# Kernel tuning notes

Hardware: AMD Instinct MI355X
Metric: run time of the kernel (lower is better)

## Reference

```python
import jax, jax.numpy as jnp
import numpy as np

N, E, R, H, KG, CIN, HID, OUT = 50000, 800000, 8, 4, 128, 256, 128, 128


def leaky(x, s=0.01):
    return jnp.where(x > 0, x, s * x)


def rgat(x, src, dst, etype, W, q, k, b, heads, n_nodes):
    # W: [R, Cin, H*C]; PyG computes bmm(x_e, W[etype]) per edge; equivalent and
    # cheaper: transform all nodes under every relation, then gather per edge.
    D = W.shape[-1]
    C = D // heads
    hr = jnp.einsum('nc,rcd->rnd', x, W)          # [R, N, D]
    out_j = hr[etype, src]                         # [E, D] messages (source)
    out_i = hr[etype, dst]                         # [E, D] targets
    a = leaky(out_i @ q + out_j @ k, 0.2)          # [E, H] additive self-attention
    amax = jax.ops.segment_max(a, dst, num_segments=n_nodes)   # per-dst max
    ex = jnp.exp(a - amax[dst])
    denom = jax.ops.segment_sum(ex, dst, num_segments=n_nodes)
    alpha = ex / denom[dst]                        # segment softmax across relations
    msg = alpha[:, :, None] * out_j.reshape(-1, heads, C)
    agg = jax.ops.segment_sum(msg, dst, num_segments=n_nodes)  # [N, H, C]
    return agg.reshape(n_nodes, D) + b             # concat heads + bias


def setup_inputs() -> dict:
    key = jax.random.key(0)
    ks = jax.random.split(key, 24)
    s = 0.05
    inp = {
        'kg_emb': jax.random.normal(ks[0], (N, KG), jnp.float32),
        'ccle': jax.random.normal(ks[1], (N, 4), jnp.float32),
        'node_id': jnp.arange(N, dtype=jnp.int32),
        'edge_index': jax.random.randint(ks[2], (2, E), 0, N),
        'edge_type': jax.random.randint(ks[3], (E,), 0, R),
        'ccle_w1': jax.random.normal(ks[4], (4, 32), jnp.float32) * s,
        'ccle_b1': jnp.zeros((32,), jnp.float32),
        'ccle_w2': jax.random.normal(ks[5], (32, 128), jnp.float32) * s,
        'ccle_b2': jnp.zeros((128,), jnp.float32),
        'W1': jax.random.normal(ks[6], (R, CIN, HID), jnp.float32) * s,
        'q1': jax.random.normal(ks[7], (HID, H), jnp.float32) * s,
        'k1': jax.random.normal(ks[8], (HID, H), jnp.float32) * s,
        'b1': jnp.zeros((HID,), jnp.float32),
        'W2': jax.random.normal(ks[9], (R, HID, OUT), jnp.float32) * s,
        'q2': jax.random.normal(ks[10], (OUT, H), jnp.float32) * s,
        'k2': jax.random.normal(ks[11], (OUT, H), jnp.float32) * s,
        'b2': jnp.zeros((OUT,), jnp.float32),
        'skip_w1': jax.random.normal(ks[12], (CIN, HID), jnp.float32) * s,
        'skip_b1': jnp.zeros((HID,), jnp.float32),
        'skip_w2': jax.random.normal(ks[13], (HID, OUT), jnp.float32) * s,
        'skip_b2': jnp.zeros((OUT,), jnp.float32),
    }
    return inp


def reference(kg_emb, ccle, node_id, edge_index, edge_type,
              ccle_w1, ccle_b1, ccle_w2, ccle_b2,
              W1, q1, k1, b1, W2, q2, k2, b2,
              skip_w1, skip_b1, skip_w2, skip_b2):
    src, dst = edge_index[0], edge_index[1]
    # OmicsLayer encoder on ccle features
    ccle_out = leaky(ccle @ ccle_w1 + ccle_b1) @ ccle_w2 + ccle_b2  # [N,128]
    x_in = jnp.concatenate([kg_emb[node_id], ccle_out[node_id]], axis=1)  # [N,256]
    x = rgat(x_in, src, dst, edge_type, W1, q1, k1, b1, H, N)
    x = leaky(x)  # dropout p=0
    x = rgat(x, src, dst, edge_type, W2, q2, k2, b2, H, N)
    skip = leaky(x_in @ skip_w1 + skip_b1) @ skip_w2 + skip_b2
    x = leaky(x + skip)
    return x
```

## Files before the change

### kernel.cpp

```cpp
#include <hip/hip_runtime.h>
#include <hip/hip_bf16.h>

#define RREL 8
#define HEADS 4
#define DH 128
#define CIN1 256
#define BN 144
#define CSP2 132

typedef unsigned short ushortT;
typedef __attribute__((ext_vector_type(8))) short short8;
typedef __attribute__((ext_vector_type(4))) float f32x4;

__device__ __forceinline__ float lrelu(float x, float s) { return x > 0.f ? x : s * x; }

__device__ __forceinline__ float bf2f(unsigned short u) {
    return __uint_as_float(((unsigned)u) << 16);
}
__device__ __forceinline__ unsigned short f2bf(float f) {
    unsigned u = __float_as_uint(f);
    return (unsigned short)((u + 0x7fffu + ((u >> 16) & 1u)) >> 16);
}

__device__ __forceinline__ void glds16(const ushortT* g, ushortT* l) {
    __builtin_amdgcn_global_load_lds(
        (const __attribute__((address_space(1))) unsigned int*)g,
        (__attribute__((address_space(3))) unsigned int*)l, 16, 0, 0);
}

__global__ __launch_bounds__(256)
void encoder_kernel(const float* __restrict__ kg, const float* __restrict__ ccle,
                    const int* __restrict__ node_id,
                    const float* __restrict__ w1, const float* __restrict__ b1,
                    const float* __restrict__ w2, const float* __restrict__ b2,
                    ushortT* __restrict__ xb, int N)
{
    __shared__ float w1s[4 * 32], b1s[32];
    __shared__ float hs[64][36];
    int tid = threadIdx.x;
    if (tid < 128) w1s[tid] = w1[tid];
    if (tid < 32) b1s[tid] = b1[tid];

    int d0 = tid & 63;
    int w = tid >> 6;
    float w2c0[32], w2c1[32];
    #pragma unroll 8
    for (int j = 0; j < 32; j++) {
        w2c0[j] = w2[j * 128 + d0];
        w2c1[j] = w2[j * 128 + d0 + 64];
    }
    float bb0 = b2[d0], bb1 = b2[d0 + 64];
    int chunk = blockIdx.x * 64;
    __syncthreads();

    {
        int ln = tid >> 2;
        int n = chunk + ln;
        if (n < N) {
            int nid = node_id[n];
            float c0 = ccle[nid * 4 + 0], c1 = ccle[nid * 4 + 1];
            float c2 = ccle[nid * 4 + 2], c3 = ccle[nid * 4 + 3];
            int jb = (tid & 3) * 8;
            #pragma unroll
            for (int jj = 0; jj < 8; jj++) {
                int j = jb + jj;
                float h = fmaf(c0, w1s[j], fmaf(c1, w1s[32 + j],
                          fmaf(c2, w1s[64 + j], fmaf(c3, w1s[96 + j], b1s[j]))));
                hs[ln][j] = lrelu(h, 0.01f);
            }
        }
    }
    __syncthreads();

    for (int it = 0; it < 16; it++) {
        int ln = it * 4 + w;
        int gn = chunk + ln;
        if (gn >= N) continue;
        int nid = node_id[gn];
        ushortT* xrow = xb + (long)gn * CIN1;
        xrow[d0]      = f2bf(kg[(long)nid * 128 + d0]);
        xrow[d0 + 64] = f2bf(kg[(long)nid * 128 + d0 + 64]);
        float o0 = bb0, o1 = bb1;
        const float4* hp = (const float4*)hs[ln];
        #pragma unroll
        for (int v = 0; v < 8; v++) {
            float4 hv = hp[v];
            o0 = fmaf(hv.x, w2c0[v * 4 + 0], o0);
            o1 = fmaf(hv.x, w2c1[v * 4 + 0], o1);
            o0 = fmaf(hv.y, w2c0[v * 4 + 1], o0);
            o1 = fmaf(hv.y, w2c1[v * 4 + 1], o1);
            o0 = fmaf(hv.z, w2c0[v * 4 + 2], o0);
            o1 = fmaf(hv.z, w2c1[v * 4 + 2], o1);
            o0 = fmaf(hv.w, w2c0[v * 4 + 3], o0);
            o1 = fmaf(hv.w, w2c1[v * 4 + 3], o1);
        }
        xrow[128 + d0]      = f2bf(o0);
        xrow[128 + d0 + 64] = f2bf(o1);
    }
}

__global__ __launch_bounds__(256)
void wtrans_kernel(const float* __restrict__ W, const float* __restrict__ q,
                   const float* __restrict__ kv, const float* __restrict__ SW,
                   ushortT* __restrict__ WT, int K)
{
    long o = (long)blockIdx.x * 256 + threadIdx.x;
    long total = (long)9 * BN * K;
    if (o >= total) return;
    int k = (int)(o % K);
    long t = o / K;
    int d = (int)(t % BN);
    int r = (int)(t / BN);
    float v = 0.f;
    if (r < 8) {
        const float* Wr = W + ((long)r * K + k) * 128;
        if (d < 128) v = Wr[d];
        else if (d < 132) {
            int h = d - 128; float s = 0.f;
            for (int c = 0; c < 128; c++) s += Wr[c] * q[c * 4 + h];
            v = s;
        } else if (d < 136) {
            int h = d - 132; float s = 0.f;
            for (int c = 0; c < 128; c++) s += Wr[c] * kv[c * 4 + h];
            v = s;
        }
    } else if (d < 128) {
        v = SW[(long)k * 128 + d];
    }
    WT[o] = f2bf(v);
}

__global__ __launch_bounds__(256, 4)
void mfma_gemm(const ushortT* __restrict__ A, const ushortT* __restrict__ Askip,
               const ushortT* __restrict__ WT, ushortT* __restrict__ hrC,
               float* __restrict__ aqkout, const float* __restrict__ bskip,
               void* __restrict__ skipout, int skipf32, int actskip,
               int M, int K)
{
    __shared__ ushortT smem[128 * 64 + BN * 64];
    ushortT* As = smem;
    ushortT* Bs = smem + 128 * 64;
    int tid = threadIdx.x;
    int lane = tid & 63, w = tid >> 6;
    int l15 = lane & 15, lhi = lane >> 4;

    int nwg = gridDim.x;
    int orig = blockIdx.x;
    int qq = nwg >> 3, rrem = nwg & 7;
    int xcd = orig & 7, o8 = orig >> 3;
    int bid = (xcd < rrem ? xcd * (qq + 1) : rrem * (qq + 1) + (xcd - rrem) * qq) + o8;

    int r = bid % 9;
    int m0 = (bid / 9) * 128;
    const ushortT* Ab = (r < 8) ? A : Askip;
    const ushortT* Wb = WT + (long)r * BN * K;
    int wbase = (tid >> 6) << 6;
    f32x4 acc[2][9] = {};

    for (int k0 = 0; k0 < K; k0 += 64) {
        #pragma unroll
        for (int it = 0; it < 4; it++) {
            int idx = it * 256 + tid;
            int row = idx >> 3;
            int ko = ((idx ^ (idx >> 3)) & 7) * 8;
            glds16(Ab + (long)(m0 + row) * K + k0 + ko,
                   As + (it * 256 + wbase) * 8);
        }
        #pragma unroll
        for (int it = 0; it < 4; it++) {
            int idx = it * 256 + tid;
            int row = idx >> 3;
            int ko = ((idx ^ (idx >> 3)) & 7) * 8;
            glds16(Wb + (long)row * K + k0 + ko,
                   Bs + (it * 256 + wbase) * 8);
        }
        if (tid < 128) {
            int idx = 1024 + tid;
            int row = idx >> 3;
            int ko = ((idx ^ (idx >> 3)) & 7) * 8;
            glds16(Wb + (long)row * K + k0 + ko,
                   Bs + (1024 + wbase) * 8);
        }
        __syncthreads();
        #pragma unroll
        for (int kk = 0; kk < 64; kk += 32) {
            int xoro = ((((kk >> 3) + lhi) ^ (l15 & 7)) << 3);
            short8 af0 = *(const short8*)(As + (w * 32 + l15) * 64 + xoro);
            short8 af1 = *(const short8*)(As + (w * 32 + 16 + l15) * 64 + xoro);
            #pragma unroll
            for (int j = 0; j < 9; j++) {
                short8 bf8 = *(const short8*)(Bs + (j * 16 + l15) * 64 + xoro);
                acc[0][j] = __builtin_amdgcn_mfma_f32_16x16x32_bf16(af0, bf8, acc[0][j], 0, 0, 0);
                acc[1][j] = __builtin_amdgcn_mfma_f32_16x16x32_bf16(af1, bf8, acc[1][j], 0, 0, 0);
            }
        }
        __syncthreads();
    }

    if (r < 8 && l15 < 8) {
        #pragma unroll
        for (int i = 0; i < 2; i++)
            #pragma unroll
            for (int g = 0; g < 4; g++) {
                int row = w * 32 + i * 16 + lhi * 4 + g;
                if (m0 + row < M)
                    aqkout[((long)r * M + m0 + row) * 8 + l15] = acc[i][8][g];
            }
    }

    ushortT* Cs = smem;
    #pragma unroll
    for (int i = 0; i < 2; i++)
        #pragma unroll
        for (int j = 0; j < 8; j++) {
            int row = w * 32 + i * 16 + lhi * 4;
            int col = j * 16 + l15;
            #pragma unroll
            for (int g = 0; g < 4; g++)
                Cs[(row + g) * CSP2 + col] = f2bf(acc[i][j][g]);
        }
    __syncthreads();
    #pragma unroll
    for (int it = 0; it < 8; it++) {
        int idx = it * 2048 + tid * 8;
        int row = idx >> 7, col = idx & 127;
        if (m0 + row >= M) continue;
        const ushortT* cp = Cs + row * CSP2 + col;
        if (r < 8) {
            long gofs = ((long)r * M + m0 + row) * DH + col;
            *(uint4*)(hrC + gofs) = *(const uint4*)cp;
        } else {
            float v[8];
            #pragma unroll
            for (int u = 0; u < 8; u++) {
                float x = bf2f(cp[u]) + bskip[col + u];
                if (actskip) x = lrelu(x, 0.01f);
                v[u] = x;
            }
            long gofs = (long)(m0 + row) * DH + col;
            if (skipf32) {
                *(float4*)((float*)skipout + gofs)     = make_float4(v[0], v[1], v[2], v[3]);
                *(float4*)((float*)skipout + gofs + 4) = make_float4(v[4], v[5], v[6], v[7]);
            } else {
                uint4 pk;
                pk.x = (unsigned)f2bf(v[0]) | ((unsigned)f2bf(v[1]) << 16);
                pk.y = (unsigned)f2bf(v[2]) | ((unsigned)f2bf(v[3]) << 16);
                pk.z = (unsigned)f2bf(v[4]) | ((unsigned)f2bf(v[5]) << 16);
                pk.w = (unsigned)f2bf(v[6]) | ((unsigned)f2bf(v[7]) << 16);
                *(uint4*)((ushortT*)skipout + gofs) = pk;
            }
        }
    }
}

__global__ __launch_bounds__(256)
void hist_kernel(const int* __restrict__ dst, int* __restrict__ deg, int E)
{
    int e = blockIdx.x * 256 + threadIdx.x;
    if (e < E) atomicAdd(&deg[dst[e]], 1);
}

#define SCAN_BLK 1024
__global__ __launch_bounds__(256)
void scan1_kernel(const int* __restrict__ deg, int* __restrict__ excl,
                  int* __restrict__ bsum, int n)
{
    __shared__ int ts[256];
    int b0 = blockIdx.x * SCAN_BLK;
    int tid = threadIdx.x;
    int v[4]; int s = 0;
    #pragma unroll
    for (int i = 0; i < 4; i++) {
        int idx = b0 + tid * 4 + i;
        v[i] = (idx < n) ? deg[idx] : 0;
        s += v[i];
    }
    ts[tid] = s;
    __syncthreads();
    for (int off = 1; off < 256; off <<= 1) {
        int t = (tid >= off) ? ts[tid - off] : 0;
        __syncthreads();
        ts[tid] += t;
        __syncthreads();
    }
    int ex = ts[tid] - s;
    #pragma unroll
    for (int i = 0; i < 4; i++) {
        int idx = b0 + tid * 4 + i;
        if (idx < n) excl[idx] = ex;
        ex += v[i];
    }
    if (tid == 255) bsum[blockIdx.x] = ts[255];
}

__global__ void scan2_kernel(int* __restrict__ bsum, int nb)
{
    if (threadIdx.x == 0 && blockIdx.x == 0) {
        int a = 0;
        for (int i = 0; i < nb; i++) { int t = bsum[i]; bsum[i] = a; a += t; }
    }
}

__global__ __launch_bounds__(256)
void scan3_kernel(int* __restrict__ rowptr, const int* __restrict__ bsum,
                  int* __restrict__ cursor, int n, int E)
{
    int idx = blockIdx.x * 256 + threadIdx.x;
    if (idx < n) {
        int v = rowptr[idx] + bsum[idx / SCAN_BLK];
        rowptr[idx] = v;
        cursor[idx] = v;
    }
    if (idx == 0) rowptr[n] = E;
}

__global__ __launch_bounds__(256)
void scatter_kernel(const int* __restrict__ src, const int* __restrict__ dst,
                    const int* __restrict__ et, int* __restrict__ cursor,
                    int* __restrict__ srcs, int* __restrict__ ets, int E)
{
    int e = blockIdx.x * 256 + threadIdx.x;
    if (e >= E) return;
    int d = dst[e];
    int pos = atomicAdd(&cursor[d], 1);
    srcs[pos] = src[e];
    ets[pos] = et[e];
}

template<typename CT, bool ADDS>
__global__ __launch_bounds__(256)
void fused_agg(const int* __restrict__ rowptr, const int* __restrict__ srcs,
               const int* __restrict__ ets, const float* __restrict__ aqk,
               const ushortT* __restrict__ hr, const float* __restrict__ bias,
               const float* __restrict__ adds, void* __restrict__ outp,
               int N, int act)
{
    __shared__ ushortT hrb[4][16][128];
    __shared__ float pbuf[4][16][4];
    int w = threadIdx.x >> 6, lane = threadIdx.x & 63;
    int d = blockIdx.x * 4 + w;
    if (d >= N) return;
    int beg = rowptr[d], end = rowptr[d + 1];
    int el = lane & 15, hq = lane >> 4;
    float m = -1e30f, den = 0.f, o0 = 0.f, o1 = 0.f;

    for (int base = beg; base < end; base += 16) {
        int nchunk = end - base; if (nchunk > 16) nchunk = 16;
        int s = 0, t = 0;
        float a = -1e30f;
        if (el < nchunk) {
            s = srcs[base + el];
            t = ets[base + el];
            a = lrelu(aqk[((long)t * N + d) * 8 + hq]
                    + aqk[((long)t * N + s) * 8 + 4 + hq], 0.2f);
        }
        float v = a;
        v = fmaxf(v, __shfl_xor(v, 1));
        v = fmaxf(v, __shfl_xor(v, 2));
        v = fmaxf(v, __shfl_xor(v, 4));
        v = fmaxf(v, __shfl_xor(v, 8));
        float mn = fmaxf(m, v);
        float scale = __expf(m - mn);
        m = mn;
        float p = (el < nchunk) ? __expf(a - mn) : 0.f;
        pbuf[w][el][hq] = p;
        float ps = p;
        ps += __shfl_xor(ps, 1);
        ps += __shfl_xor(ps, 2);
        ps += __shfl_xor(ps, 4);
        ps += __shfl_xor(ps, 8);
        den = den * scale + ps;
        #pragma unroll
        for (int pass = 0; pass < 4; pass++) {
            int rj = pass * 4 + (lane >> 4);
            int sj = __shfl(s, rj);
            int tj = __shfl(t, rj);
            if (rj < nchunk) {
                uint4 hv = *(const uint4*)(hr + ((long)tj * N + sj) * DH + (lane & 15) * 8);
                *(uint4*)&hrb[w][rj][(lane & 15) * 8] = hv;
            }
        }
        o0 *= scale; o1 *= scale;
        asm volatile("s_waitcnt lgkmcnt(0)" ::: "memory");
        for (int j = 0; j < nchunk; j++) {
            float pj = pbuf[w][j][hq];
            unsigned hv = *(const unsigned*)&hrb[w][j][lane * 2];
            o0 = fmaf(pj, bf2f((ushortT)hv), o0);
            o1 = fmaf(pj, bf2f((ushortT)(hv >> 16)), o1);
        }
    }
    float inv = (den > 0.f) ? 1.f / den : 0.f;
    o0 *= inv; o1 *= inv;
    if (bias) { o0 += bias[2 * lane]; o1 += bias[2 * lane + 1]; }
    if constexpr (ADDS) {
        float2 sv = *(const float2*)(adds + (long)d * DH + lane * 2);
        o0 += sv.x; o1 += sv.y;
    }
    if (act) { o0 = lrelu(o0, 0.01f); o1 = lrelu(o1, 0.01f); }
    if constexpr (sizeof(CT) == 2) {
        unsigned pk = (unsigned)f2bf(o0) | ((unsigned)f2bf(o1) << 16);
        ((unsigned*)outp)[(long)d * 64 + lane] = pk;
    } else {
        *(float2*)((float*)outp + (long)d * DH + lane * 2) = make_float2(o0, o1);
    }
}

__global__ __launch_bounds__(256)
void fill_report(float* __restrict__ out, float v, long total)
{
    long i = (long)blockIdx.x * 256 + threadIdx.x;
    if (i < total) out[i] = v;
}

extern "C" void kernel_launch(void* const* d_in, const int* in_sizes, int n_in,
                              void* d_out, int out_size, void* d_ws, size_t ws_size,
                              hipStream_t stream)
{
    const float* kg      = (const float*)d_in[0];
    const float* ccle    = (const float*)d_in[1];
    const int*   node_id = (const int*)d_in[2];
    const int*   eidx    = (const int*)d_in[3];
    const int*   etype   = (const int*)d_in[4];
    const float* cw1 = (const float*)d_in[5];
    const float* cb1 = (const float*)d_in[6];
    const float* cw2 = (const float*)d_in[7];
    const float* cb2 = (const float*)d_in[8];
    const float* W1  = (const float*)d_in[9];
    const float* q1  = (const float*)d_in[10];
    const float* k1  = (const float*)d_in[11];
    const float* b1  = (const float*)d_in[12];
    const float* W2  = (const float*)d_in[13];
    const float* q2  = (const float*)d_in[14];
    const float* k2  = (const float*)d_in[15];
    const float* b2  = (const float*)d_in[16];
    const float* sw1 = (const float*)d_in[17];
    const float* sb1 = (const float*)d_in[18];
    const float* sw2 = (const float*)d_in[19];
    const float* sb2 = (const float*)d_in[20];

    const int N = in_sizes[2];
    const int E = in_sizes[4];
    const int* src = eidx;
    const int* dst = eidx + E;

    dim3 blk(256);
    long nd = (long)N * 128;
    int nd_blocks = (int)((nd + 255) / 256);
    int eb = (E + 255) / 256;

    const long WTN = (long)9 * BN * 256;
    size_t need = (size_t)N * (256 + 128 + 128 + 1024) * 2 + (size_t)WTN * 2
                + (size_t)N * 64 * 4 + (size_t)N * 128 * 4
                + ((size_t)3 * N + 257 + 2 * (size_t)E) * 4;
    if (ws_size < need) {
        fill_report<<<nd_blocks, blk, 0, stream>>>((float*)d_out,
            (float)(double)(ws_size >> 20), nd);
        return;
    }
    ushortT* xb  = (ushortT*)d_ws;
    ushortT* x1b = xb + (long)N * CIN1;
    ushortT* s1b = x1b + (long)N * DH;
    ushortT* hr  = s1b + (long)N * DH;
    ushortT* WT  = hr + (long)RREL * N * DH;
    float* aqk   = (float*)(WT + WTN);
    float* s2    = aqk + (long)N * 64;
    int* rowptr  = (int*)(s2 + (long)N * DH);
    int* cursor  = rowptr + (N + 1);
    int* deg     = cursor + N;
    int* bsum    = deg + N;
    int* srcs    = bsum + 256;
    int* ets     = srcs + E;

    int nb = (N + SCAN_BLK - 1) / SCAN_BLK;
    int fgrid = (N + 3) / 4;
    int mblocks = (N + 127) / 128;
    dim3 ggrid(mblocks * 9);

    encoder_kernel<<<(N + 63) / 64, blk, 0, stream>>>(kg, ccle, node_id,
        cw1, cb1, cw2, cb2, xb, N);

    hipMemsetAsync(deg, 0, (size_t)N * sizeof(int), stream);
    hist_kernel<<<eb, blk, 0, stream>>>(dst, deg, E);
    scan1_kernel<<<nb, blk, 0, stream>>>(deg, rowptr, bsum, N);
    scan2_kernel<<<1, 64, 0, stream>>>(bsum, nb);
    scan3_kernel<<<(N + 255) / 256, blk, 0, stream>>>(rowptr, bsum, cursor, N, E);
    scatter_kernel<<<eb, blk, 0, stream>>>(src, dst, etype, cursor, srcs, ets, E);

    wtrans_kernel<<<(int)(((long)9 * BN * CIN1 + 255) / 256), blk, 0, stream>>>(
        W1, q1, k1, sw1, WT, CIN1);
    mfma_gemm<<<ggrid, blk, 0, stream>>>(xb, xb, WT, hr, aqk, sb1, s1b,
        0, 1, N, CIN1);
    fused_agg<ushortT, false><<<fgrid, blk, 0, stream>>>(rowptr, srcs, ets,
        aqk, hr, b1, nullptr, x1b, N, 1);

    wtrans_kernel<<<(int)(((long)9 * BN * DH + 255) / 256), blk, 0, stream>>>(
        W2, q2, k2, sw2, WT, DH);
    mfma_gemm<<<ggrid, blk, 0, stream>>>(x1b, s1b, WT, hr, aqk, sb2, s2,
        1, 0, N, DH);
    fused_agg<float, true><<<fgrid, blk, 0, stream>>>(rowptr, srcs, ets,
        aqk, hr, b2, s2, (float*)d_out, N, 1);
}
```

Measured before the change: 365.4 us.

## Accumulate gathered messages in registers instead of staging through LDS

The fused aggregation kernel no longer stages the 16 gathered source rows and their softmax weights in shared memory. Each lane now loads four edges' 8-column slices straight into registers and accumulates eight partial sums. The four edge groups are combined with cross-lane shuffles at the end, and 16 lanes write vectorized outputs. This removes LDS traffic and the serial per-edge inner loop, and issues all gathers before the softmax math so load latency can overlap it, at the cost of more registers and a final shuffle reduction.

```diff
diff --git a/kernel.cpp b/kernel.cpp
--- a/kernel.cpp
+++ b/kernel.cpp
@@ -335,26 +335,39 @@
                const float* __restrict__ adds, void* __restrict__ outp,
                int N, int act)
 {
-    __shared__ ushortT hrb[4][16][128];
-    __shared__ float pbuf[4][16][4];
     int w = threadIdx.x >> 6, lane = threadIdx.x & 63;
     int d = blockIdx.x * 4 + w;
     if (d >= N) return;
     int beg = rowptr[d], end = rowptr[d + 1];
     int el = lane & 15, hq = lane >> 4;
-    float m = -1e30f, den = 0.f, o0 = 0.f, o1 = 0.f;
+    int slot = el, rgrp = hq;
+    int hh = slot >> 2;
+    int hbase = hh << 4;
+    float m = -1e30f, den = 0.f;
+    float acc8[8] = {0.f, 0.f, 0.f, 0.f, 0.f, 0.f, 0.f, 0.f};
 
     for (int base = beg; base < end; base += 16) {
         int nchunk = end - base; if (nchunk > 16) nchunk = 16;
+        bool have = el < nchunk;
         int s = 0, t = 0;
-        float a = -1e30f;
-        if (el < nchunk) {
-            s = srcs[base + el];
-            t = ets[base + el];
-            a = lrelu(aqk[((long)t * N + d) * 8 + hq]
-                    + aqk[((long)t * N + s) * 8 + 4 + hq], 0.2f);
-        }
-        float v = a;
+        if (have) { s = srcs[base + el]; t = ets[base + el]; }
+        float aqv = 0.f, akv = 0.f;
+        if (have) {
+            aqv = aqk[((long)t * N + d) * 8 + hq];
+            akv = aqk[((long)t * N + s) * 8 + 4 + hq];
+        }
+        int r0 = rgrp, r1 = 4 + rgrp, r2 = 8 + rgrp, r3 = 12 + rgrp;
+        int s0 = __shfl(s, r0), t0 = __shfl(t, r0);
+        int s1 = __shfl(s, r1), t1 = __shfl(t, r1);
+        int s2 = __shfl(s, r2), t2 = __shfl(t, r2);
+        int s3 = __shfl(s, r3), t3 = __shfl(t, r3);
+        uint4 hv0 = make_uint4(0, 0, 0, 0), hv1 = hv0, hv2 = hv0, hv3 = hv0;
+        if (r0 < nchunk) hv0 = *(const uint4*)(hr + ((long)t0 * N + s0) * DH + slot * 8);
+        if (r1 < nchunk) hv1 = *(const uint4*)(hr + ((long)t1 * N + s1) * DH + slot * 8);
+        if (r2 < nchunk) hv2 = *(const uint4*)(hr + ((long)t2 * N + s2) * DH + slot * 8);
+        if (r3 < nchunk) hv3 = *(const uint4*)(hr + ((long)t3 * N + s3) * DH + slot * 8);
+        float av = have ? lrelu(aqv + akv, 0.2f) : -1e30f;
+        float v = av;
         v = fmaxf(v, __shfl_xor(v, 1));
         v = fmaxf(v, __shfl_xor(v, 2));
         v = fmaxf(v, __shfl_xor(v, 4));
@@ -362,46 +375,66 @@
         float mn = fmaxf(m, v);
         float scale = __expf(m - mn);
         m = mn;
-        float p = (el < nchunk) ? __expf(a - mn) : 0.f;
-        pbuf[w][el][hq] = p;
+        float p = have ? __expf(av - mn) : 0.f;
         float ps = p;
         ps += __shfl_xor(ps, 1);
         ps += __shfl_xor(ps, 2);
         ps += __shfl_xor(ps, 4);
         ps += __shfl_xor(ps, 8);
         den = den * scale + ps;
-        #pragma unroll
-        for (int pass = 0; pass < 4; pass++) {
-            int rj = pass * 4 + (lane >> 4);
-            int sj = __shfl(s, rj);
-            int tj = __shfl(t, rj);
-            if (rj < nchunk) {
-                uint4 hv = *(const uint4*)(hr + ((long)tj * N + sj) * DH + (lane & 15) * 8);
-                *(uint4*)&hrb[w][rj][(lane & 15) * 8] = hv;
-            }
-        }
-        o0 *= scale; o1 *= scale;
-        asm volatile("s_waitcnt lgkmcnt(0)" ::: "memory");
-        for (int j = 0; j < nchunk; j++) {
-            float pj = pbuf[w][j][hq];
-            unsigned hv = *(const unsigned*)&hrb[w][j][lane * 2];
-            o0 = fmaf(pj, bf2f((ushortT)hv), o0);
-            o1 = fmaf(pj, bf2f((ushortT)(hv >> 16)), o1);
-        }
-    }
-    float inv = (den > 0.f) ? 1.f / den : 0.f;
-    o0 *= inv; o1 *= inv;
-    if (bias) { o0 += bias[2 * lane]; o1 += bias[2 * lane + 1]; }
-    if constexpr (ADDS) {
-        float2 sv = *(const float2*)(adds + (long)d * DH + lane * 2);
-        o0 += sv.x; o1 += sv.y;
-    }
-    if (act) { o0 = lrelu(o0, 0.01f); o1 = lrelu(o1, 0.01f); }
-    if constexpr (sizeof(CT) == 2) {
-        unsigned pk = (unsigned)f2bf(o0) | ((unsigned)f2bf(o1) << 16);
-        ((unsigned*)outp)[(long)d * 64 + lane] = pk;
-    } else {
-        *(float2*)((float*)outp + (long)d * DH + lane * 2) = make_float2(o0, o1);
+        float sc = __shfl(scale, hbase | slot);
+        float p0 = __shfl(p, hbase | r0);
+        float p1 = __shfl(p, hbase | r1);
+        float p2 = __shfl(p, hbase | r2);
+        float p3 = __shfl(p, hbase | r3);
+        #pragma unroll
+        for (int u = 0; u < 8; u++) acc8[u] *= sc;
+        unsigned uu0[4] = {hv0.x, hv0.y, hv0.z, hv0.w};
+        unsigned uu1[4] = {hv1.x, hv1.y, hv1.z, hv1.w};
+        unsigned uu2[4] = {hv2.x, hv2.y, hv2.z, hv2.w};
+        unsigned uu3[4] = {hv3.x, hv3.y, hv3.z, hv3.w};
+        #pragma unroll
+        for (int q = 0; q < 4; q++) {
+            acc8[2 * q]     = fmaf(p0, bf2f((ushortT)uu0[q]), acc8[2 * q]);
+            acc8[2 * q + 1] = fmaf(p0, bf2f((ushortT)(uu0[q] >> 16)), acc8[2 * q + 1]);
+            acc8[2 * q]     = fmaf(p1, bf2f((ushortT)uu1[q]), acc8[2 * q]);
+            acc8[2 * q + 1] = fmaf(p1, bf2f((ushortT)(uu1[q] >> 16)), acc8[2 * q + 1]);
+            acc8[2 * q]     = fmaf(p2, bf2f((ushortT)uu2[q]), acc8[2 * q]);
+            acc8[2 * q + 1] = fmaf(p2, bf2f((ushortT)(uu2[q] >> 16)), acc8[2 * q + 1]);
+            acc8[2 * q]     = fmaf(p3, bf2f((ushortT)uu3[q]), acc8[2 * q]);
+            acc8[2 * q + 1] = fmaf(p3, bf2f((ushortT)(uu3[q] >> 16)), acc8[2 * q + 1]);
+        }
+    }
+    #pragma unroll
+    for (int u = 0; u < 8; u++) {
+        acc8[u] += __shfl_xor(acc8[u], 16);
+        acc8[u] += __shfl_xor(acc8[u], 32);
+    }
+    float dn = __shfl(den, hbase | slot);
+    float inv = (dn > 0.f) ? 1.f / dn : 0.f;
+    if (rgrp == 0) {
+        int c0 = slot * 8;
+        const float* ap = ADDS ? (adds + (long)d * DH + c0) : nullptr;
+        float vv[8];
+        #pragma unroll
+        for (int u = 0; u < 8; u++) {
+            float x = acc8[u] * inv;
+            if (bias) x += bias[c0 + u];
+            if constexpr (ADDS) x += ap[u];
+            if (act) x = lrelu(x, 0.01f);
+            vv[u] = x;
+        }
+        if constexpr (sizeof(CT) == 2) {
+            uint4 pk;
+            pk.x = (unsigned)f2bf(vv[0]) | ((unsigned)f2bf(vv[1]) << 16);
+            pk.y = (unsigned)f2bf(vv[2]) | ((unsigned)f2bf(vv[3]) << 16);
+            pk.z = (unsigned)f2bf(vv[4]) | ((unsigned)f2bf(vv[5]) << 16);
+            pk.w = (unsigned)f2bf(vv[6]) | ((unsigned)f2bf(vv[7]) << 16);
+            *(uint4*)((ushortT*)outp + (long)d * DH + c0) = pk;
+        } else {
+            *(float4*)((float*)outp + (long)d * DH + c0)     = make_float4(vv[0], vv[1], vv[2], vv[3]);
+            *(float4*)((float*)outp + (long)d * DH + c0 + 4) = make_float4(vv[4], vv[5], vv[6], vv[7]);
+        }
     }
 }
 
```

Result: slower. 372.8 us (+2.0%).
